# Optimization experiments

Measured on AMD Instinct MI355X. Metric: run time of the kernel, lower is better.

Reference implementation:

```python
import jax, jax.numpy as jnp
import numpy as np

B, L = 4, 2048
D_MODEL, D_INNER, D_STATE, DT_RANK, K = 512, 1024, 16, 64, 4


def setup_inputs() -> dict:
    key = jax.random.key(0)
    ks = jax.random.split(key, 21)
    def n(k, shape, s=0.02):
        return (jax.random.normal(k, shape) * s).astype(jnp.float32)
    inp = {"x": jax.random.normal(ks[0], (B, L, D_MODEL), jnp.float32)}
    for i, sfx in enumerate(("f", "b")):
        o = 1 + i * 8
        inp[f"W_in_{sfx}"] = n(ks[o], (2 * D_INNER, D_MODEL))
        inp[f"conv_w_{sfx}"] = n(ks[o + 1], (D_INNER, 1, K), 0.1)
        inp[f"conv_b_{sfx}"] = jnp.zeros((D_INNER,), jnp.float32)
        inp[f"A_log_{sfx}"] = (jax.random.normal(ks[o + 2], (D_STATE, D_INNER)) * 0.1).astype(jnp.float32)
        inp[f"D_{sfx}"] = jnp.ones((D_INNER,), jnp.float32)
        inp[f"Wx_{sfx}"] = n(ks[o + 3], (DT_RANK + 2 * D_STATE, D_INNER))
        inp[f"Wdt_{sfx}"] = n(ks[o + 4], (D_INNER, DT_RANK), DT_RANK ** -0.5)
        dt = jnp.exp(jax.random.uniform(ks[o + 5], (D_INNER,)) * (np.log(0.1) - np.log(0.001)) + np.log(0.001))
        inp[f"bdt_{sfx}"] = (dt + jnp.log(-jnp.expm1(-dt))).astype(jnp.float32)
        inp[f"Wout_{sfx}"] = n(ks[o + 6], (D_MODEL, D_INNER))
    return inp


def _mamba_block(x, W_in, conv_w, conv_b, A_log, Dp, Wx, Wdt, bdt, Wout):
    # x: [B, L, d_model]
    xz = jnp.einsum('bld,ed->ble', x, W_in)              # [B, L, 2*d_inner]
    xb, zb = xz[..., :D_INNER], xz[..., D_INNER:]
    # causal depthwise conv over time
    xc = jnp.transpose(xb, (0, 2, 1))                     # [B, M, L]
    xc = jax.lax.conv_general_dilated(
        xc, conv_w, window_strides=(1,), padding=[(K - 1, 0)],
        feature_group_count=D_INNER,
        dimension_numbers=('NCH', 'OIH', 'NCH')) + conv_b[None, :, None]
    xb = jax.nn.silu(jnp.transpose(xc, (0, 2, 1)))        # [B, L, M]
    # input-dependent SSM parameters
    proj = jnp.einsum('blm,pm->blp', xb, Wx)              # [B, L, dt_rank+2D]
    dt_in = proj[..., :DT_RANK]
    Bs = proj[..., DT_RANK:DT_RANK + D_STATE]             # [B, L, D]
    Cs = proj[..., DT_RANK + D_STATE:]                    # [B, L, D]
    dt = jax.nn.softplus(jnp.einsum('blr,mr->blm', dt_in, Wdt) + bdt)  # [B, L, M]
    A_T = -jnp.exp(A_log).T                               # [M, D]

    def step(h, inp):
        dt_t, x_t, B_t, C_t = inp                         # [B,M],[B,M],[B,D],[B,D]
        dA = jnp.exp(dt_t[:, :, None] * A_T[None])        # [B, M, D]
        h = dA * h + (dt_t * x_t)[:, :, None] * B_t[:, None, :]
        y_t = jnp.einsum('bmd,bd->bm', h, C_t)
        return h, y_t

    xs = (jnp.moveaxis(dt, 1, 0), jnp.moveaxis(xb, 1, 0),
          jnp.moveaxis(Bs, 1, 0), jnp.moveaxis(Cs, 1, 0))
    h0 = jnp.zeros((x.shape[0], D_INNER, D_STATE), x.dtype)
    _, ys = jax.lax.scan(step, h0, xs)                    # [L, B, M]
    y = jnp.moveaxis(ys, 0, 1) + Dp * xb                  # [B, L, M]
    y = y * jax.nn.silu(zb)                               # SiLU gate
    return jnp.einsum('blm,dm->bld', y, Wout)             # [B, L, d_model]


def reference(x,
              W_in_f, conv_w_f, conv_b_f, A_log_f, D_f, Wx_f, Wdt_f, bdt_f, Wout_f,
              W_in_b, conv_w_b, conv_b_b, A_log_b, D_b, Wx_b, Wdt_b, bdt_b, Wout_b):
    out_f = _mamba_block(x, W_in_f, conv_w_f, conv_b_f, A_log_f, D_f, Wx_f, Wdt_f, bdt_f, Wout_f)
    out_b = jnp.flip(_mamba_block(jnp.flip(x, 1), W_in_b, conv_w_b, conv_b_b, A_log_b, D_b, Wx_b, Wdt_b, bdt_b, Wout_b), 1)
    return out_f + out_b
```

## Files before the change

kernel.cpp:

```cpp
#include <hip/hip_runtime.h>
#include <hip/hip_bf16.h>
#include <cstdint>
#include <cstdio>

typedef float f32x4 __attribute__((ext_vector_type(4)));
typedef short s16x8 __attribute__((ext_vector_type(8)));

__device__ __forceinline__ float us2f(unsigned short u){
  union { unsigned int i; float f; } v; v.i = ((unsigned int)u) << 16; return v.f;
}
__device__ __forceinline__ unsigned short f2us(float f){
  union { float f; unsigned int i; } v; v.f = f;
  unsigned int r = v.i + 0x7fffu + ((v.i >> 16) & 1u);
  return (unsigned short)(r >> 16);
}
__device__ __forceinline__ void gload_lds16(const void* g, void* l){
  __builtin_amdgcn_global_load_lds(
      (const __attribute__((address_space(1))) unsigned int*)g,
      (__attribute__((address_space(3))) unsigned int*)l, 16, 0, 0);
}

__global__ __launch_bounds__(256)
void prep_k(const float* __restrict__ x,
            const float* __restrict__ W_in_f, const float* __restrict__ W_in_b,
            const float* __restrict__ Wx_f,   const float* __restrict__ Wx_b,
            const float* __restrict__ Wdt_f,  const float* __restrict__ Wdt_b,
            const float* __restrict__ Wout_f, const float* __restrict__ Wout_b,
            const float* __restrict__ Alog_f, const float* __restrict__ Alog_b,
            const float* __restrict__ bdt_f,  const float* __restrict__ bdt_b,
            unsigned short* __restrict__ W1cat, unsigned short* __restrict__ Wxpad,
            unsigned short* __restrict__ Wdtb,  unsigned short* __restrict__ Woutcat,
            float* __restrict__ A2, float* __restrict__ bdtcat,
            unsigned short* __restrict__ xbf)
{
  long i = (long)blockIdx.x * 256 + threadIdx.x;
  if (i < 4194304) {
    xbf[i] = f2us(x[i]); return;
  }
  i -= 4194304;
  if (i < 2097152) {
    int n = (int)(i >> 9), k = (int)(i & 511);
    float v = (n < 2048) ? W_in_f[(long)n*512 + k] : W_in_b[(long)(n-2048)*512 + k];
    W1cat[i] = f2us(v); return;
  }
  i -= 2097152;
  if (i < 262144) {
    int dir = (int)(i >> 17); long r = i & 131071; int n = (int)(r >> 10), k = (int)(r & 1023);
    const float* Wx = dir ? Wx_b : Wx_f;
    Wxpad[(long)dir*131072 + r] = f2us(n < 96 ? Wx[(long)n*1024 + k] : 0.f); return;
  }
  i -= 262144;
  if (i < 131072) {
    int dir = (int)(i >> 16); long r = i & 65535;
    Wdtb[i] = f2us((dir ? Wdt_b : Wdt_f)[r]); return;
  }
  i -= 131072;
  if (i < 1048576) {
    int n = (int)(i >> 11), k = (int)(i & 2047);
    float v = (k < 1024) ? Wout_f[(long)n*1024 + k] : Wout_b[(long)n*1024 + (k-1024)];
    Woutcat[i] = f2us(v); return;
  }
  i -= 1048576;
  if (i < 32768) {
    int dir = (int)(i >> 14); long r = i & 16383; int m = (int)(r >> 4), d = (int)(r & 15);
    const float* Al = dir ? Alog_b : Alog_f;
    A2[i] = -__expf(Al[(long)d*1024 + m]) * 1.4426950408889634f; return;
  }
  i -= 32768;
  if (i < 2048) {
    int dir = (int)(i >> 10), m = (int)(i & 1023);
    bdtcat[i] = (dir ? bdt_b : bdt_f)[m]; return;
  }
}

template<int OUT_MODE>
__global__ __launch_bounds__(256)
void gemm_bt(const unsigned short* __restrict__ Ap, const unsigned short* __restrict__ Bp,
             void* __restrict__ Cp, const float* __restrict__ biasp,
             int K, int lda, int ldb, int ldc,
             long az, long bz, long cz, int biasz)
{
  const int z   = blockIdx.z;
  const int tid = threadIdx.x;
  const int bm  = blockIdx.x, bn = blockIdx.y;

  __shared__ __align__(16) unsigned short Ash[128][32];
  __shared__ __align__(16) unsigned short Bsh[128][32];

  const int wave = tid >> 6, lane = tid & 63;
  const int wr = (wave >> 1) << 6, wc = (wave & 1) << 6;
  const int fr = lane & 15, fs = lane >> 4;

  const int r0 = tid >> 2;
  const int sg = tid & 3, kofs = sg << 3;

  const unsigned short* Ag = Ap + (long)z * az;
  const unsigned short* Bg = Bp + (long)z * bz;

  const long aoff0 = (long)(bm*128 + r0)*lda + kofs;
  const long aoff1 = aoff0 + (long)64*lda;
  const long boff0 = (long)(bn*128 + r0)*ldb + kofs;
  const long boff1 = boff0 + (long)64*ldb;

  unsigned short* lA0 = &Ash[r0][kofs];
  unsigned short* lA1 = &Ash[64 + r0][kofs];
  unsigned short* lB0 = &Bsh[r0][kofs];
  unsigned short* lB1 = &Bsh[64 + r0][kofs];

  f32x4 acc[4][4];
  #pragma unroll
  for (int i=0;i<4;i++)
    #pragma unroll
    for (int j=0;j<4;j++) acc[i][j] = (f32x4){0.f,0.f,0.f,0.f};

  const int NK = K >> 5;
  for (int ks = 0; ks < NK; ++ks){
    const long k0 = (long)ks << 5;
    __syncthreads();
    gload_lds16(Ag + aoff0 + k0, lA0);
    gload_lds16(Ag + aoff1 + k0, lA1);
    gload_lds16(Bg + boff0 + k0, lB0);
    gload_lds16(Bg + boff1 + k0, lB1);
    __syncthreads();

    s16x8 af[4], bfv[4];
    #pragma unroll
    for (int i=0;i<4;i++){
      af[i]  = *(const s16x8*)&Ash[wr + i*16 + fr][fs << 3];
      bfv[i] = *(const s16x8*)&Bsh[wc + i*16 + fr][fs << 3];
    }
    #pragma unroll
    for (int i=0;i<4;i++)
      #pragma unroll
      for (int j=0;j<4;j++)
        acc[i][j] = __builtin_amdgcn_mfma_f32_16x16x32_bf16(af[i], bfv[j], acc[i][j], 0, 0, 0);
  }

  #pragma unroll
  for (int i=0;i<4;i++){
    const int rowb = bm*128 + wr + i*16 + (fs << 2);
    #pragma unroll
    for (int j=0;j<4;j++){
      const int col = bn*128 + wc + j*16 + fr;
      #pragma unroll
      for (int e=0;e<4;e++){
        float v = acc[i][j][e];
        const long cidx = (long)z*cz + (long)(rowb + e)*ldc + col;
        if (OUT_MODE == 2){
          ((float*)Cp)[cidx] = v;
        } else if (OUT_MODE == 1){
          v += biasp[z*biasz + col];
          v = fmaxf(v, 0.f) + log1pf(__expf(-fabsf(v)));
          ((unsigned short*)Cp)[cidx] = f2us(v);
        } else {
          ((unsigned short*)Cp)[cidx] = f2us(v);
        }
      }
    }
  }
}

__global__ __launch_bounds__(256)
void conv_silu_k(const unsigned short* __restrict__ xz,
                 const float* __restrict__ wf, const float* __restrict__ cbf,
                 const float* __restrict__ wb, const float* __restrict__ cbb,
                 unsigned short* __restrict__ xbc)
{
  const int tid = threadIdx.x;
  const long tok = blockIdx.x;
  const int l   = (int)(tok & 2047);
  const int dir = tid >> 7;
  const int mg  = (tid & 127) << 3;
  const float* w  = dir ? wb  : wf;
  const float* cb = dir ? cbb : cbf;
  const long rowb = tok << 12;
  const int  xcol = (dir << 11) + mg;

  f32x4 wv[8];
  #pragma unroll
  for (int e=0;e<8;e++) wv[e] = *(const f32x4*)(w + (mg + e)*4);
  const f32x4 cb0 = *(const f32x4*)(cb + mg);
  const f32x4 cb1 = *(const f32x4*)(cb + mg + 4);

  float acc[8];
  #pragma unroll
  for (int e=0;e<4;e++){ acc[e]=cb0[e]; acc[4+e]=cb1[e]; }

  #pragma unroll
  for (int k=0;k<4;k++){
    const int off = dir ? (3 - k) : (k - 3);
    const int pos = l + off;
    if (pos >= 0 && pos < 2048){
      const s16x8 xv = *(const s16x8*)(xz + rowb + ((long)off << 12) + xcol);
      #pragma unroll
      for (int e=0;e<8;e++)
        acc[e] = __builtin_fmaf(wv[e][k], us2f((unsigned short)xv[e]), acc[e]);
    }
  }
  s16x8 out;
  #pragma unroll
  for (int e=0;e<8;e++){
    const float s = acc[e] / (1.f + __expf(-acc[e]));
    out[e] = (short)f2us(s);
  }
  *(s16x8*)(xbc + tok*2048 + (dir << 10) + mg) = out;
}

#define SCHUNK 64
#define NCHUNK 32

__global__ __launch_bounds__(256)
void scan1_k(const unsigned short* __restrict__ dtb, const unsigned short* __restrict__ xbc,
             const unsigned short* __restrict__ proj, const float* __restrict__ A2,
             float* __restrict__ hloc, float* __restrict__ Ssum)
{
  const int tidx = threadIdx.x;
  const int cb = blockIdx.x, c = blockIdx.y, bz = blockIdx.z;
  const int b = bz >> 1, dir = bz & 1;
  const int m = cb*256 + tidx;

  float a2[16];
  { const f32x4* p = (const f32x4*)(A2 + (((long)dir*1024 + m) << 4));
    f32x4 v0=p[0], v1=p[1], v2=p[2], v3=p[3];
    #pragma unroll
    for (int e=0;e<4;e++){ a2[e]=v0[e]; a2[4+e]=v1[e]; a2[8+e]=v2[e]; a2[12+e]=v3[e]; } }

  __shared__ float Bs[SCHUNK][16];
  if (tidx < 128){
    const int t = tidx >> 1, half = tidx & 1;
    const int l = dir ? (2047 - (c*SCHUNK + t)) : (c*SCHUNK + t);
    const long tok = (long)b*2048 + l;
    const s16x8 v = *(const s16x8*)(proj + (long)dir*1048576 + tok*128 + 64 + half*8);
    #pragma unroll
    for (int e=0;e<8;e++) Bs[t][half*8 + e] = us2f((unsigned short)v[e]);
  }
  __syncthreads();

  const int  l0 = dir ? (2047 - c*SCHUNK) : (c*SCHUNK);
  const int  ls = dir ? -1 : 1;
  const long tok0 = (long)b*2048 + l0;
  const unsigned short* dtp = dtb + (((long)dir) << 23) + tok0*1024 + m;
  const unsigned short* xvp = xbc + tok0*2048 + (dir << 10) + m;
  const long dstp = (long)ls*1024, xstp = (long)ls*2048;

  float h[16];
  #pragma unroll
  for (int d=0;d<16;d++) h[d]=0.f;
  float S = 0.f;

  unsigned short du = *dtp, xu = *xvp;
  for (int t=0;t<SCHUNK;t++){
    const float dt = us2f(du), xv = us2f(xu);
    dtp += dstp; xvp += xstp;
    du = *dtp; xu = *xvp;
    S += dt;
    const float u = dt * xv;
    const f32x4* bp = (const f32x4*)&Bs[t][0];
    f32x4 bv0=bp[0], bv1=bp[1], bv2=bp[2], bv3=bp[3];
    #pragma unroll
    for (int d=0;d<16;d++){
      const float bval = (d<4)? bv0[d&3] : (d<8)? bv1[d&3] : (d<12)? bv2[d&3] : bv3[d&3];
      const float a = __builtin_amdgcn_exp2f(dt * a2[d]);
      h[d] = __builtin_fmaf(a, h[d], u * bval);
    }
  }
  const long o = ((((long)bz * NCHUNK) + c)*1024 + m);
  f32x4* Hp = (f32x4*)(hloc + (o << 4));
  #pragma unroll
  for (int q=0;q<4;q++){
    f32x4 hv;
    #pragma unroll
    for (int e=0;e<4;e++) hv[e]=h[q*4+e];
    Hp[q]=hv;
  }
  Ssum[o] = S;
}

__global__ __launch_bounds__(256)
void scan2_k(const float* __restrict__ A2, const float* __restrict__ Ssum,
             float* __restrict__ hloc)
{
  const long idx = (long)blockIdx.x*256 + threadIdx.x;
  const long bz = idx >> 14; const int r = (int)(idx & 16383);
  const int dir = (int)(bz & 1);
  const float a2 = A2[((long)dir << 14) + r];
  const long base = bz * NCHUNK;
  float hs = 0.f;
  float hlN = hloc[base*16384 + r];
  float SN  = Ssum[base*1024 + (r >> 4)];
  for (int c=0;c<NCHUNK;c++){
    const float hl = hlN, Sv = SN;
    const int cn = (c+1 < NCHUNK) ? c+1 : c;
    hlN = hloc[(base+cn)*16384 + r];
    SN  = Ssum[(base+cn)*1024 + (r >> 4)];
    const float P = __builtin_amdgcn_exp2f(a2 * Sv);
    hloc[(base+c)*16384 + r] = hs;
    hs = __builtin_fmaf(P, hs, hl);
  }
}

__global__ __launch_bounds__(256)
void scan3_k(const unsigned short* __restrict__ dtb, const unsigned short* __restrict__ xbc,
             const unsigned short* __restrict__ proj, const float* __restrict__ A2,
             const float* __restrict__ hstart, const unsigned short* __restrict__ xz,
             const float* __restrict__ D_f, const float* __restrict__ D_b,
             unsigned short* __restrict__ ybuf)
{
  const int tidx = threadIdx.x;
  const int cb = blockIdx.x, c = blockIdx.y, bz = blockIdx.z;
  const int b = bz >> 1, dir = bz & 1;
  const int m = cb*256 + tidx;

  float a2[16];
  { const f32x4* p = (const f32x4*)(A2 + (((long)dir*1024 + m) << 4));
    f32x4 v0=p[0], v1=p[1], v2=p[2], v3=p[3];
    #pragma unroll
    for (int e=0;e<4;e++){ a2[e]=v0[e]; a2[4+e]=v1[e]; a2[8+e]=v2[e]; a2[12+e]=v3[e]; } }
  const float Dm = (dir ? D_b : D_f)[m];

  __shared__ float Bs[SCHUNK][16];
  __shared__ float Cs[SCHUNK][16];
  {
    const int half = tidx & 1;
    if (tidx < 128){
      const int t = tidx >> 1;
      const int l = dir ? (2047 - (c*SCHUNK + t)) : (c*SCHUNK + t);
      const long tok = (long)b*2048 + l;
      const s16x8 vb = *(const s16x8*)(proj + (long)dir*1048576 + tok*128 + 64 + half*8);
      #pragma unroll
      for (int e=0;e<8;e++) Bs[t][half*8+e] = us2f((unsigned short)vb[e]);
    } else {
      const int t = (tidx - 128) >> 1;
      const int l = dir ? (2047 - (c*SCHUNK + t)) : (c*SCHUNK + t);
      const long tok = (long)b*2048 + l;
      const s16x8 vc = *(const s16x8*)(proj + (long)dir*1048576 + tok*128 + 80 + half*8);
      #pragma unroll
      for (int e=0;e<8;e++) Cs[t][half*8+e] = us2f((unsigned short)vc[e]);
    }
  }

  float h[16];
  { const long o = ((((long)bz*NCHUNK) + c)*1024 + m) << 4;
    const f32x4* p = (const f32x4*)(hstart + o);
    f32x4 v0=p[0], v1=p[1], v2=p[2], v3=p[3];
    #pragma unroll
    for (int e=0;e<4;e++){ h[e]=v0[e]; h[4+e]=v1[e]; h[8+e]=v2[e]; h[12+e]=v3[e]; } }
  __syncthreads();

  const int  l0 = dir ? (2047 - c*SCHUNK) : (c*SCHUNK);
  const int  ls = dir ? -1 : 1;
  const long tok0 = (long)b*2048 + l0;
  const unsigned short* dtp = dtb + (((long)dir) << 23) + tok0*1024 + m;
  const unsigned short* xvp = xbc + tok0*2048 + (dir << 10) + m;
  const unsigned short* zp  = xz  + (tok0 << 12) + (dir << 11) + 1024 + m;
  unsigned short*       yp  = ybuf + tok0*2048 + (dir << 10) + m;
  const long dstp = (long)ls*1024, xstp = (long)ls*2048, zstp = (long)ls << 12;

  unsigned short du = *dtp, xu = *xvp, zu = *zp;
  for (int t=0;t<SCHUNK;t++){
    const float dt = us2f(du), xv = us2f(xu), zb = us2f(zu);
    dtp += dstp; xvp += xstp; zp += zstp;
    du = *dtp; xu = *xvp; zu = *zp;
    const float u = dt * xv;
    const f32x4* bp = (const f32x4*)&Bs[t][0];
    const f32x4* cp = (const f32x4*)&Cs[t][0];
    f32x4 bv0=bp[0], bv1=bp[1], bv2=bp[2], bv3=bp[3];
    f32x4 cv0=cp[0], cv1=cp[1], cv2=cp[2], cv3=cp[3];
    float y0=0.f, y1=0.f, y2=0.f, y3=0.f;
    #pragma unroll
    for (int d=0;d<16;d++){
      const float bval = (d<4)? bv0[d&3] : (d<8)? bv1[d&3] : (d<12)? bv2[d&3] : bv3[d&3];
      const float cval = (d<4)? cv0[d&3] : (d<8)? cv1[d&3] : (d<12)? cv2[d&3] : cv3[d&3];
      const float a = __builtin_amdgcn_exp2f(dt * a2[d]);
      h[d] = __builtin_fmaf(a, h[d], u * bval);
      if (d<4)       y0 = __builtin_fmaf(h[d], cval, y0);
      else if (d<8)  y1 = __builtin_fmaf(h[d], cval, y1);
      else if (d<12) y2 = __builtin_fmaf(h[d], cval, y2);
      else           y3 = __builtin_fmaf(h[d], cval, y3);
    }
    float y = ((y0+y1)+(y2+y3)) + Dm * xv;
    const float gate = zb / (1.f + __expf(-zb));
    *yp = f2us(y * gate);
    yp += xstp;
  }
}

extern "C" void kernel_launch(void* const* d_in, const int* in_sizes, int n_in,
                              void* d_out, int out_size, void* d_ws, size_t ws_size,
                              hipStream_t stream)
{
  const float* x      = (const float*)d_in[0];
  const float* W_in_f = (const float*)d_in[1];
  const float* convw_f= (const float*)d_in[2];
  const float* convb_f= (const float*)d_in[3];
  const float* Alog_f = (const float*)d_in[4];
  const float* D_f    = (const float*)d_in[5];
  const float* Wx_f   = (const float*)d_in[6];
  const float* Wdt_f  = (const float*)d_in[7];
  const float* bdt_f  = (const float*)d_in[8];
  const float* Wout_f = (const float*)d_in[9];
  const float* W_in_b = (const float*)d_in[10];
  const float* convw_b= (const float*)d_in[11];
  const float* convb_b= (const float*)d_in[12];
  const float* Alog_b = (const float*)d_in[13];
  const float* D_b    = (const float*)d_in[14];
  const float* Wx_b   = (const float*)d_in[15];
  const float* Wdt_b  = (const float*)d_in[16];
  const float* bdt_b  = (const float*)d_in[17];
  const float* Wout_b = (const float*)d_in[18];

  char* w = (char*)d_ws;
  auto carve = [&](size_t bytes) -> char* {
    char* p = w; w += (bytes + 255) & ~(size_t)255; return p;
  };
  unsigned short* W1cat   = (unsigned short*)carve(4096ULL*512*2);
  unsigned short* Wxpad   = (unsigned short*)carve(2ULL*128*1024*2);
  unsigned short* Wdtb    = (unsigned short*)carve(2ULL*1024*64*2);
  unsigned short* Woutcat = (unsigned short*)carve(512ULL*2048*2);
  float*          A2      = (float*)carve(2ULL*1024*16*4);
  float*          bdtcat  = (float*)carve(2048ULL*4);
  unsigned short* xz      = (unsigned short*)carve(8192ULL*4096*2);
  unsigned short* xbc     = (unsigned short*)carve(8192ULL*2048*2);
  unsigned short* proj    = (unsigned short*)carve(2ULL*8192*128*2);
  unsigned short* dtb     = (unsigned short*)carve(2ULL*8192*1024*2);
  unsigned short* ybuf    = (unsigned short*)carve(8192ULL*2048*2);
  float*          hloc    = (float*)carve(8ULL*NCHUNK*1024*16*4);
  float*          Ssum    = (float*)carve(8ULL*NCHUNK*1024*4);
  unsigned short* xbf     = ybuf;

  if ((size_t)(w - (char*)d_ws) > ws_size) {
    fprintf(stderr, "kernel_launch: ws too small (%zu needed, %zu given)\n",
            (size_t)(w - (char*)d_ws), ws_size);
    return;
  }

  prep_k<<<dim3(30344), 256, 0, stream>>>(x, W_in_f, W_in_b, Wx_f, Wx_b, Wdt_f, Wdt_b,
                                          Wout_f, Wout_b, Alog_f, Alog_b, bdt_f, bdt_b,
                                          W1cat, Wxpad, Wdtb, Woutcat, A2, bdtcat, xbf);
  gemm_bt<0><<<dim3(64,32,1), 256, 0, stream>>>(xbf, W1cat, xz, nullptr,
                                                512, 512, 512, 4096, 0, 0, 0, 0);
  conv_silu_k<<<dim3(8192), 256, 0, stream>>>(xz, convw_f, convb_f, convw_b, convb_b, xbc);
  gemm_bt<0><<<dim3(64,1,2), 256, 0, stream>>>(xbc, Wxpad, proj, nullptr,
                                               1024, 2048, 1024, 128,
                                               1024, 131072, 1048576, 0);
  gemm_bt<1><<<dim3(64,8,2), 256, 0, stream>>>(proj, Wdtb, dtb, bdtcat,
                                               64, 128, 64, 1024,
                                               1048576, 65536, 8388608, 1024);
  scan1_k<<<dim3(4,NCHUNK,8), 256, 0, stream>>>(dtb, xbc, proj, A2, hloc, Ssum);
  scan2_k<<<dim3(512), 256, 0, stream>>>(A2, Ssum, hloc);
  scan3_k<<<dim3(4,NCHUNK,8), 256, 0, stream>>>(dtb, xbc, proj, A2, hloc, xz, D_f, D_b, ybuf);
  gemm_bt<2><<<dim3(64,4,1), 256, 0, stream>>>(ybuf, Woutcat, d_out, nullptr,
                                               2048, 2048, 2048, 512, 0, 0, 0, 0);
}
```

Before: 347.8 us.

## Process two channels per scan thread, halve chunk length, store chunk states in bf16

Scan kernels now handle two adjacent channels per thread with 32-bit packed loads and stores, so the grid in the channel dimension is halved. Chunk length drops from 64 to 32 and the chunk count doubles from 32 to 64, which shortens each thread's serial loop but makes the scan2 carry pass longer. The intermediate chunk states in hloc are stored as bf16 instead of fp32 to cut the traffic between the three scan stages. This costs precision in the carried states and doubles register use for state per thread, which may lower occupancy.

```diff
diff --git a/kernel.cpp b/kernel.cpp
--- a/kernel.cpp
+++ b/kernel.cpp
@@ -4,6 +4,7 @@
 #include <cstdio>
 
 typedef float f32x4 __attribute__((ext_vector_type(4)));
+typedef float f32x2 __attribute__((ext_vector_type(2)));
 typedef short s16x8 __attribute__((ext_vector_type(8)));
 
 __device__ __forceinline__ float us2f(unsigned short u){
@@ -206,27 +207,29 @@
   *(s16x8*)(xbc + tok*2048 + (dir << 10) + mg) = out;
 }
 
-#define SCHUNK 64
-#define NCHUNK 32
+#define SCHUNK 32
+#define NCHUNK 64
 
 __global__ __launch_bounds__(256)
 void scan1_k(const unsigned short* __restrict__ dtb, const unsigned short* __restrict__ xbc,
              const unsigned short* __restrict__ proj, const float* __restrict__ A2,
-             float* __restrict__ hloc, float* __restrict__ Ssum)
+             unsigned short* __restrict__ hloc, float* __restrict__ Ssum)
 {
   const int tidx = threadIdx.x;
   const int cb = blockIdx.x, c = blockIdx.y, bz = blockIdx.z;
   const int b = bz >> 1, dir = bz & 1;
-  const int m = cb*256 + tidx;
-
-  float a2[16];
-  { const f32x4* p = (const f32x4*)(A2 + (((long)dir*1024 + m) << 4));
-    f32x4 v0=p[0], v1=p[1], v2=p[2], v3=p[3];
-    #pragma unroll
-    for (int e=0;e<4;e++){ a2[e]=v0[e]; a2[4+e]=v1[e]; a2[8+e]=v2[e]; a2[12+e]=v3[e]; } }
+  const int p  = cb*256 + tidx;
+  const int m0 = p << 1;
+
+  float a20[16], a21[16];
+  { const f32x4* q0 = (const f32x4*)(A2 + (((long)dir*1024 + m0) << 4));
+    #pragma unroll
+    for (int q=0;q<4;q++){ f32x4 v0=q0[q], v1=q0[q+4];
+      #pragma unroll
+      for (int e=0;e<4;e++){ a20[q*4+e]=v0[e]; a21[q*4+e]=v1[e]; } } }
 
   __shared__ float Bs[SCHUNK][16];
-  if (tidx < 128){
+  if (tidx < 64){
     const int t = tidx >> 1, half = tidx & 1;
     const int l = dir ? (2047 - (c*SCHUNK + t)) : (c*SCHUNK + t);
     const long tok = (long)b*2048 + l;
@@ -239,46 +242,49 @@
   const int  l0 = dir ? (2047 - c*SCHUNK) : (c*SCHUNK);
   const int  ls = dir ? -1 : 1;
   const long tok0 = (long)b*2048 + l0;
-  const unsigned short* dtp = dtb + (((long)dir) << 23) + tok0*1024 + m;
-  const unsigned short* xvp = xbc + tok0*2048 + (dir << 10) + m;
+  const unsigned short* dtp = dtb + (((long)dir) << 23) + tok0*1024 + m0;
+  const unsigned short* xvp = xbc + tok0*2048 + (dir << 10) + m0;
   const long dstp = (long)ls*1024, xstp = (long)ls*2048;
 
-  float h[16];
-  #pragma unroll
-  for (int d=0;d<16;d++) h[d]=0.f;
-  float S = 0.f;
-
-  unsigned short du = *dtp, xu = *xvp;
+  float h0[16], h1[16];
+  #pragma unroll
+  for (int d=0;d<16;d++){ h0[d]=0.f; h1[d]=0.f; }
+  float S0 = 0.f, S1 = 0.f;
+
+  unsigned int du = *(const unsigned int*)dtp, xu = *(const unsigned int*)xvp;
   for (int t=0;t<SCHUNK;t++){
-    const float dt = us2f(du), xv = us2f(xu);
+    const float dt0 = us2f((unsigned short)(du & 0xffff)), dt1 = us2f((unsigned short)(du >> 16));
+    const float x0  = us2f((unsigned short)(xu & 0xffff)), x1  = us2f((unsigned short)(xu >> 16));
     dtp += dstp; xvp += xstp;
-    du = *dtp; xu = *xvp;
-    S += dt;
-    const float u = dt * xv;
+    du = *(const unsigned int*)dtp; xu = *(const unsigned int*)xvp;
+    S0 += dt0; S1 += dt1;
+    const float u0 = dt0 * x0, u1 = dt1 * x1;
     const f32x4* bp = (const f32x4*)&Bs[t][0];
     f32x4 bv0=bp[0], bv1=bp[1], bv2=bp[2], bv3=bp[3];
     #pragma unroll
     for (int d=0;d<16;d++){
       const float bval = (d<4)? bv0[d&3] : (d<8)? bv1[d&3] : (d<12)? bv2[d&3] : bv3[d&3];
-      const float a = __builtin_amdgcn_exp2f(dt * a2[d]);
-      h[d] = __builtin_fmaf(a, h[d], u * bval);
-    }
-  }
-  const long o = ((((long)bz * NCHUNK) + c)*1024 + m);
-  f32x4* Hp = (f32x4*)(hloc + (o << 4));
-  #pragma unroll
-  for (int q=0;q<4;q++){
-    f32x4 hv;
-    #pragma unroll
-    for (int e=0;e<4;e++) hv[e]=h[q*4+e];
-    Hp[q]=hv;
-  }
-  Ssum[o] = S;
+      const float e0 = __builtin_amdgcn_exp2f(dt0 * a20[d]);
+      const float e1 = __builtin_amdgcn_exp2f(dt1 * a21[d]);
+      h0[d] = __builtin_fmaf(e0, h0[d], u0 * bval);
+      h1[d] = __builtin_fmaf(e1, h1[d], u1 * bval);
+    }
+  }
+  const long o = ((((long)bz * NCHUNK) + c)*1024 + m0) << 4;
+  s16x8 hv[4];
+  #pragma unroll
+  for (int q=0;q<2;q++)
+    #pragma unroll
+    for (int e=0;e<8;e++){ hv[q][e]   = (short)f2us(h0[q*8+e]);
+                           hv[q+2][e] = (short)f2us(h1[q*8+e]); }
+  #pragma unroll
+  for (int q=0;q<4;q++) *(s16x8*)(hloc + o + q*8) = hv[q];
+  *(f32x2*)(Ssum + ((((long)bz * NCHUNK) + c)*1024 + m0)) = (f32x2){S0, S1};
 }
 
 __global__ __launch_bounds__(256)
 void scan2_k(const float* __restrict__ A2, const float* __restrict__ Ssum,
-             float* __restrict__ hloc)
+             unsigned short* __restrict__ hloc)
 {
   const long idx = (long)blockIdx.x*256 + threadIdx.x;
   const long bz = idx >> 14; const int r = (int)(idx & 16383);
@@ -286,15 +292,15 @@
   const float a2 = A2[((long)dir << 14) + r];
   const long base = bz * NCHUNK;
   float hs = 0.f;
-  float hlN = hloc[base*16384 + r];
+  float hlN = us2f(hloc[base*16384 + r]);
   float SN  = Ssum[base*1024 + (r >> 4)];
   for (int c=0;c<NCHUNK;c++){
     const float hl = hlN, Sv = SN;
     const int cn = (c+1 < NCHUNK) ? c+1 : c;
-    hlN = hloc[(base+cn)*16384 + r];
+    hlN = us2f(hloc[(base+cn)*16384 + r]);
     SN  = Ssum[(base+cn)*1024 + (r >> 4)];
     const float P = __builtin_amdgcn_exp2f(a2 * Sv);
-    hloc[(base+c)*16384 + r] = hs;
+    hloc[(base+c)*16384 + r] = f2us(hs);
     hs = __builtin_fmaf(P, hs, hl);
   }
 }
@@ -302,85 +308,97 @@
 __global__ __launch_bounds__(256)
 void scan3_k(const unsigned short* __restrict__ dtb, const unsigned short* __restrict__ xbc,
              const unsigned short* __restrict__ proj, const float* __restrict__ A2,
-             const float* __restrict__ hstart, const unsigned short* __restrict__ xz,
+             const unsigned short* __restrict__ hstart, const unsigned short* __restrict__ xz,
              const float* __restrict__ D_f, const float* __restrict__ D_b,
              unsigned short* __restrict__ ybuf)
 {
   const int tidx = threadIdx.x;
   const int cb = blockIdx.x, c = blockIdx.y, bz = blockIdx.z;
   const int b = bz >> 1, dir = bz & 1;
-  const int m = cb*256 + tidx;
-
-  float a2[16];
-  { const f32x4* p = (const f32x4*)(A2 + (((long)dir*1024 + m) << 4));
-    f32x4 v0=p[0], v1=p[1], v2=p[2], v3=p[3];
-    #pragma unroll
-    for (int e=0;e<4;e++){ a2[e]=v0[e]; a2[4+e]=v1[e]; a2[8+e]=v2[e]; a2[12+e]=v3[e]; } }
-  const float Dm = (dir ? D_b : D_f)[m];
+  const int p  = cb*256 + tidx;
+  const int m0 = p << 1;
+
+  float a20[16], a21[16];
+  { const f32x4* q0 = (const f32x4*)(A2 + (((long)dir*1024 + m0) << 4));
+    #pragma unroll
+    for (int q=0;q<4;q++){ f32x4 v0=q0[q], v1=q0[q+4];
+      #pragma unroll
+      for (int e=0;e<4;e++){ a20[q*4+e]=v0[e]; a21[q*4+e]=v1[e]; } } }
+  const float* Dp = dir ? D_b : D_f;
+  const float Dm0 = Dp[m0], Dm1 = Dp[m0+1];
 
   __shared__ float Bs[SCHUNK][16];
   __shared__ float Cs[SCHUNK][16];
-  {
+  if (tidx < 128){
     const int half = tidx & 1;
-    if (tidx < 128){
-      const int t = tidx >> 1;
-      const int l = dir ? (2047 - (c*SCHUNK + t)) : (c*SCHUNK + t);
-      const long tok = (long)b*2048 + l;
+    const int t = (tidx & 63) >> 1;
+    const int l = dir ? (2047 - (c*SCHUNK + t)) : (c*SCHUNK + t);
+    const long tok = (long)b*2048 + l;
+    if (tidx < 64){
       const s16x8 vb = *(const s16x8*)(proj + (long)dir*1048576 + tok*128 + 64 + half*8);
       #pragma unroll
       for (int e=0;e<8;e++) Bs[t][half*8+e] = us2f((unsigned short)vb[e]);
     } else {
-      const int t = (tidx - 128) >> 1;
-      const int l = dir ? (2047 - (c*SCHUNK + t)) : (c*SCHUNK + t);
-      const long tok = (long)b*2048 + l;
       const s16x8 vc = *(const s16x8*)(proj + (long)dir*1048576 + tok*128 + 80 + half*8);
       #pragma unroll
       for (int e=0;e<8;e++) Cs[t][half*8+e] = us2f((unsigned short)vc[e]);
     }
   }
 
-  float h[16];
-  { const long o = ((((long)bz*NCHUNK) + c)*1024 + m) << 4;
-    const f32x4* p = (const f32x4*)(hstart + o);
-    f32x4 v0=p[0], v1=p[1], v2=p[2], v3=p[3];
-    #pragma unroll
-    for (int e=0;e<4;e++){ h[e]=v0[e]; h[4+e]=v1[e]; h[8+e]=v2[e]; h[12+e]=v3[e]; } }
+  float h0[16], h1[16];
+  { const long o = ((((long)bz*NCHUNK) + c)*1024 + m0) << 4;
+    s16x8 hv0 = *(const s16x8*)(hstart + o);
+    s16x8 hv1 = *(const s16x8*)(hstart + o + 8);
+    s16x8 hv2 = *(const s16x8*)(hstart + o + 16);
+    s16x8 hv3 = *(const s16x8*)(hstart + o + 24);
+    #pragma unroll
+    for (int e=0;e<8;e++){ h0[e]   = us2f((unsigned short)hv0[e]);
+                           h0[8+e] = us2f((unsigned short)hv1[e]);
+                           h1[e]   = us2f((unsigned short)hv2[e]);
+                           h1[8+e] = us2f((unsigned short)hv3[e]); } }
   __syncthreads();
 
   const int  l0 = dir ? (2047 - c*SCHUNK) : (c*SCHUNK);
   const int  ls = dir ? -1 : 1;
   const long tok0 = (long)b*2048 + l0;
-  const unsigned short* dtp = dtb + (((long)dir) << 23) + tok0*1024 + m;
-  const unsigned short* xvp = xbc + tok0*2048 + (dir << 10) + m;
-  const unsigned short* zp  = xz  + (tok0 << 12) + (dir << 11) + 1024 + m;
-  unsigned short*       yp  = ybuf + tok0*2048 + (dir << 10) + m;
+  const unsigned short* dtp = dtb + (((long)dir) << 23) + tok0*1024 + m0;
+  const unsigned short* xvp = xbc + tok0*2048 + (dir << 10) + m0;
+  const unsigned short* zp  = xz  + (tok0 << 12) + (dir << 11) + 1024 + m0;
+  unsigned short*       yp  = ybuf + tok0*2048 + (dir << 10) + m0;
   const long dstp = (long)ls*1024, xstp = (long)ls*2048, zstp = (long)ls << 12;
 
-  unsigned short du = *dtp, xu = *xvp, zu = *zp;
+  unsigned int du = *(const unsigned int*)dtp, xu = *(const unsigned int*)xvp,
+               zu = *(const unsigned int*)zp;
   for (int t=0;t<SCHUNK;t++){
-    const float dt = us2f(du), xv = us2f(xu), zb = us2f(zu);
+    const float dt0 = us2f((unsigned short)(du & 0xffff)), dt1 = us2f((unsigned short)(du >> 16));
+    const float x0  = us2f((unsigned short)(xu & 0xffff)), x1  = us2f((unsigned short)(xu >> 16));
+    const float z0  = us2f((unsigned short)(zu & 0xffff)), z1  = us2f((unsigned short)(zu >> 16));
     dtp += dstp; xvp += xstp; zp += zstp;
-    du = *dtp; xu = *xvp; zu = *zp;
-    const float u = dt * xv;
+    du = *(const unsigned int*)dtp; xu = *(const unsigned int*)xvp;
+    zu = *(const unsigned int*)zp;
+    const float u0 = dt0 * x0, u1 = dt1 * x1;
     const f32x4* bp = (const f32x4*)&Bs[t][0];
     const f32x4* cp = (const f32x4*)&Cs[t][0];
     f32x4 bv0=bp[0], bv1=bp[1], bv2=bp[2], bv3=bp[3];
     f32x4 cv0=cp[0], cv1=cp[1], cv2=cp[2], cv3=cp[3];
-    float y0=0.f, y1=0.f, y2=0.f, y3=0.f;
+    float y0a=0.f, y0b=0.f, y1a=0.f, y1b=0.f;
     #pragma unroll
     for (int d=0;d<16;d++){
       const float bval = (d<4)? bv0[d&3] : (d<8)? bv1[d&3] : (d<12)? bv2[d&3] : bv3[d&3];
       const float cval = (d<4)? cv0[d&3] : (d<8)? cv1[d&3] : (d<12)? cv2[d&3] : cv3[d&3];
-      const float a = __builtin_amdgcn_exp2f(dt * a2[d]);
-      h[d] = __builtin_fmaf(a, h[d], u * bval);
-      if (d<4)       y0 = __builtin_fmaf(h[d], cval, y0);
-      else if (d<8)  y1 = __builtin_fmaf(h[d], cval, y1);
-      else if (d<12) y2 = __builtin_fmaf(h[d], cval, y2);
-      else           y3 = __builtin_fmaf(h[d], cval, y3);
-    }
-    float y = ((y0+y1)+(y2+y3)) + Dm * xv;
-    const float gate = zb / (1.f + __expf(-zb));
-    *yp = f2us(y * gate);
+      const float e0 = __builtin_amdgcn_exp2f(dt0 * a20[d]);
+      const float e1 = __builtin_amdgcn_exp2f(dt1 * a21[d]);
+      h0[d] = __builtin_fmaf(e0, h0[d], u0 * bval);
+      h1[d] = __builtin_fmaf(e1, h1[d], u1 * bval);
+      if (d & 1){ y0b = __builtin_fmaf(h0[d], cval, y0b); y1b = __builtin_fmaf(h1[d], cval, y1b); }
+      else      { y0a = __builtin_fmaf(h0[d], cval, y0a); y1a = __builtin_fmaf(h1[d], cval, y1a); }
+    }
+    const float y0 = (y0a + y0b) + Dm0 * x0;
+    const float y1 = (y1a + y1b) + Dm1 * x1;
+    const float g0 = z0 / (1.f + __expf(-z0));
+    const float g1 = z1 / (1.f + __expf(-z1));
+    const unsigned int out = (unsigned int)f2us(y0 * g0) | ((unsigned int)f2us(y1 * g1) << 16);
+    *(unsigned int*)yp = out;
     yp += xstp;
   }
 }
@@ -424,7 +442,7 @@
   unsigned short* proj    = (unsigned short*)carve(2ULL*8192*128*2);
   unsigned short* dtb     = (unsigned short*)carve(2ULL*8192*1024*2);
   unsigned short* ybuf    = (unsigned short*)carve(8192ULL*2048*2);
-  float*          hloc    = (float*)carve(8ULL*NCHUNK*1024*16*4);
+  unsigned short* hloc    = (unsigned short*)carve(8ULL*NCHUNK*1024*16*2);
   float*          Ssum    = (float*)carve(8ULL*NCHUNK*1024*4);
   unsigned short* xbf     = ybuf;
 
@@ -446,9 +464,9 @@
   gemm_bt<1><<<dim3(64,8,2), 256, 0, stream>>>(proj, Wdtb, dtb, bdtcat,
                                                64, 128, 64, 1024,
                                                1048576, 65536, 8388608, 1024);
-  scan1_k<<<dim3(4,NCHUNK,8), 256, 0, stream>>>(dtb, xbc, proj, A2, hloc, Ssum);
+  scan1_k<<<dim3(2,NCHUNK,8), 256, 0, stream>>>(dtb, xbc, proj, A2, hloc, Ssum);
   scan2_k<<<dim3(512), 256, 0, stream>>>(A2, Ssum, hloc);
-  scan3_k<<<dim3(4,NCHUNK,8), 256, 0, stream>>>(dtb, xbc, proj, A2, hloc, xz, D_f, D_b, ybuf);
+  scan3_k<<<dim3(2,NCHUNK,8), 256, 0, stream>>>(dtb, xbc, proj, A2, hloc, xz, D_f, D_b, ybuf);
   gemm_bt<2><<<dim3(64,4,1), 256, 0, stream>>>(ybuf, Woutcat, d_out, nullptr,
                                                2048, 2048, 2048, 512, 0, 0, 0, 0);
 }
```

After: 349.2 us. Within noise of the previous version (+0.4%).
